# Optimization experiments

Hardware: AMD Instinct MI355X
Metric: run time of the kernel (lower is better)

The kernel has to match this reference:

```python
import jax, jax.numpy as jnp
import numpy as np

B = 1024
NOISE_DIM = 100
EMBED_DIM = 16
HIDDEN = 256
MAX_ORDER = 7
OUT_SIZE = (2 ** (MAX_ORDER + 1) + 1)  # 257
OUT_DIM = OUT_SIZE * OUT_SIZE           # 66049


def setup_inputs() -> dict:
    key = jax.random.key(0)
    ks = jax.random.split(key, 10)
    s = 0.02  # small init so sigmoid outputs are well-conditioned
    noise = jax.random.normal(ks[0], (B, NOISE_DIM), dtype=jnp.float32)
    # torch.stack in the original requires a homogeneous-order batch; use max order.
    orders = jnp.full((B,), MAX_ORDER, dtype=jnp.int32)
    embed_table = jax.random.normal(ks[1], (MAX_ORDER + 1, EMBED_DIM), dtype=jnp.float32)
    W1 = jax.random.normal(ks[2], (NOISE_DIM + EMBED_DIM, HIDDEN), dtype=jnp.float32) * s
    b1 = jnp.zeros((HIDDEN,), dtype=jnp.float32)
    W2 = jax.random.normal(ks[3], (HIDDEN, HIDDEN * 2), dtype=jnp.float32) * s
    b2 = jnp.zeros((HIDDEN * 2,), dtype=jnp.float32)
    W3 = jax.random.normal(ks[4], (HIDDEN * 2, HIDDEN * 4), dtype=jnp.float32) * s
    b3 = jnp.zeros((HIDDEN * 4,), dtype=jnp.float32)
    # expert head for the selected (homogeneous) order = MAX_ORDER
    W_out = jax.random.normal(ks[5], (HIDDEN * 4, OUT_DIM), dtype=jnp.float32) * s
    b_out = jnp.zeros((OUT_DIM,), dtype=jnp.float32)
    return {
        "noise": noise, "orders": orders, "embed_table": embed_table,
        "W1": W1, "b1": b1, "W2": W2, "b2": b2, "W3": W3, "b3": b3,
        "W_out": W_out, "b_out": b_out,
    }


def reference(noise, orders, embed_table, W1, b1, W2, b2, W3, b3, W_out, b_out):
    # embed(orders) -> (B, EMBED_DIM), concat with noise
    e = embed_table[orders]
    x = jnp.concatenate([noise, e], axis=1)            # (B, 116)
    h = jax.nn.relu(x @ W1 + b1)                       # (B, 256)
    h = jax.nn.relu(h @ W2 + b2)                       # (B, 512)
    h = jax.nn.relu(h @ W3 + b3)                       # (B, 1024)
    # per-order expert head; batch is homogeneous (all orders == MAX_ORDER),
    # the only configuration in which the original torch.stack succeeds.
    out = jax.nn.sigmoid(h @ W_out + b_out)            # (B, 66049)
    return out.reshape(noise.shape[0], OUT_SIZE, OUT_SIZE)
```

## Files before the change

kernel.cpp:

```cpp
#include <hip/hip_runtime.h>

typedef float f32x4 __attribute__((ext_vector_type(4)));
typedef float f32x2 __attribute__((ext_vector_type(2)));
typedef short s16x8 __attribute__((ext_vector_type(8)));

#define N_OUT 66049
#define K_DIM 1024
#define NPANEL 517

__device__ __forceinline__ ushort f2bf(float f) {
    union { float f; unsigned u; } x; x.f = f;
    unsigned r = x.u + 0x7fffu + ((x.u >> 16) & 1u);
    return (ushort)(r >> 16);
}

__device__ __forceinline__ unsigned cvt_pk_bf16(float lo, float hi) {
    unsigned r;
    asm("v_cvt_pk_bf16_f32 %0, %1, %2" : "=v"(r) : "v"(lo), "v"(hi));
    return r;
}

__device__ __forceinline__ void lds_load16(const void* g, void* l) {
    auto gp = reinterpret_cast<const __attribute__((address_space(1))) char*>(
        reinterpret_cast<uintptr_t>(g));
    auto lp = reinterpret_cast<__attribute__((address_space(3))) char*>(
        reinterpret_cast<uintptr_t>(l));
    __builtin_amdgcn_global_load_lds(gp, lp, 16, 0, 0);
}

__device__ __forceinline__ void chain_body(
    int bid, int tid, char* smem,
    const float* __restrict__ noise, const int* __restrict__ orders,
    const float* __restrict__ emb,
    const float* __restrict__ W1, const float* __restrict__ b1,
    const float* __restrict__ W2, const float* __restrict__ b2,
    const float* __restrict__ W3, const float* __restrict__ b3,
    ushort* __restrict__ h3)
{
    float* xs  = (float*)smem;
    float* h1s = (float*)(smem + 1920);
    float* h2s = (float*)(smem + 6016);
    const int R0 = bid * 4;

    for (int i = tid; i < 4 * 116; i += 256) {
        const int r = i / 116, c = i - r * 116;
        xs[r * 120 + c] = (c < 100) ? noise[(R0 + r) * 100 + c]
                                    : emb[orders[R0 + r] * 16 + (c - 100)];
    }
    __syncthreads();

    {
        const float bb = b1[tid];
        float a0 = bb, a1 = bb, a2 = bb, a3 = bb;
        #pragma unroll 4
        for (int k = 0; k < 116; ++k) {
            const float w = W1[k * 256 + tid];
            a0 = fmaf(xs[0 * 120 + k], w, a0);
            a1 = fmaf(xs[1 * 120 + k], w, a1);
            a2 = fmaf(xs[2 * 120 + k], w, a2);
            a3 = fmaf(xs[3 * 120 + k], w, a3);
        }
        h1s[0 * 256 + tid] = fmaxf(a0, 0.f);
        h1s[1 * 256 + tid] = fmaxf(a1, 0.f);
        h1s[2 * 256 + tid] = fmaxf(a2, 0.f);
        h1s[3 * 256 + tid] = fmaxf(a3, 0.f);
    }
    __syncthreads();

    {
        const f32x2 bb = *reinterpret_cast<const f32x2*>(&b2[tid * 2]);
        f32x2 a[4] = {bb, bb, bb, bb};
        for (int k = 0; k < 256; k += 4) {
            f32x4 hh[4];
            #pragma unroll
            for (int r = 0; r < 4; ++r) hh[r] = *reinterpret_cast<const f32x4*>(&h1s[r * 256 + k]);
            #pragma unroll
            for (int kk = 0; kk < 4; ++kk) {
                const f32x2 w = *reinterpret_cast<const f32x2*>(&W2[(k + kk) * 512 + tid * 2]);
                #pragma unroll
                for (int r = 0; r < 4; ++r) {
                    a[r][0] = fmaf(hh[r][kk], w[0], a[r][0]);
                    a[r][1] = fmaf(hh[r][kk], w[1], a[r][1]);
                }
            }
        }
        #pragma unroll
        for (int r = 0; r < 4; ++r) {
            h2s[r * 512 + tid * 2]     = fmaxf(a[r][0], 0.f);
            h2s[r * 512 + tid * 2 + 1] = fmaxf(a[r][1], 0.f);
        }
    }
    __syncthreads();

    {
        const f32x4 bb = *reinterpret_cast<const f32x4*>(&b3[tid * 4]);
        f32x4 a[4] = {bb, bb, bb, bb};
        for (int k = 0; k < 512; k += 4) {
            f32x4 hh[4];
            #pragma unroll
            for (int r = 0; r < 4; ++r) hh[r] = *reinterpret_cast<const f32x4*>(&h2s[r * 512 + k]);
            #pragma unroll
            for (int kk = 0; kk < 4; ++kk) {
                const f32x4 w = *reinterpret_cast<const f32x4*>(&W3[(k + kk) * 1024 + tid * 4]);
                #pragma unroll
                for (int r = 0; r < 4; ++r) {
                    a[r][0] = fmaf(hh[r][kk], w[0], a[r][0]);
                    a[r][1] = fmaf(hh[r][kk], w[1], a[r][1]);
                    a[r][2] = fmaf(hh[r][kk], w[2], a[r][2]);
                    a[r][3] = fmaf(hh[r][kk], w[3], a[r][3]);
                }
            }
        }
        #pragma unroll
        for (int r = 0; r < 4; ++r) {
            ushort4 u;
            u.x = f2bf(fmaxf(a[r][0], 0.f));
            u.y = f2bf(fmaxf(a[r][1], 0.f));
            u.z = f2bf(fmaxf(a[r][2], 0.f));
            u.w = f2bf(fmaxf(a[r][3], 0.f));
            *reinterpret_cast<ushort4*>(&h3[(size_t)(R0 + r) * 1024 + tid * 4]) = u;
        }
    }
}

__device__ __forceinline__ void convert_wout_body(
    int p, int kt, int tid, char* smem,
    const float* __restrict__ Wout, ushort* __restrict__ Bp)
{
    float* T = (float*)smem;
    const int k0 = kt * 64;

    if (p < NPANEL - 1) {
        const int c4 = (tid & 31) * 4;
        const int r0 = tid >> 5;
        const float* src = Wout + (size_t)k0 * N_OUT + (size_t)p * 128 + c4;
        #pragma unroll
        for (int i = 0; i < 8; ++i) {
            const int r = r0 + i * 8;
            f32x4 v = __builtin_nontemporal_load(
                reinterpret_cast<const f32x4*>(src + (size_t)r * N_OUT));
            *reinterpret_cast<f32x4*>(&T[r * 132 + c4]) = v;
        }
    } else {
        const int c = tid & 31, r0 = tid >> 5;
        #pragma unroll
        for (int i = 0; i < 8; ++i) {
            const int r = r0 + i * 8;
            #pragma unroll
            for (int j = 0; j < 4; ++j) {
                int col = p * 128 + c * 4 + j;
                if (col > N_OUT - 1) col = N_OUT - 1;
                T[r * 132 + c * 4 + j] = Wout[(size_t)(k0 + r) * N_OUT + col];
            }
        }
    }
    __syncthreads();

    const size_t base = ((size_t)p * 128 + kt * 8) * 128 * 8;
    #pragma unroll
    for (int i = 0; i < 4; ++i) {
        const int v = tid + i * 256;
        const int kbl = v >> 7, nl = v & 127;
        s16x8 o;
        #pragma unroll
        for (int j = 0; j < 8; ++j) o[j] = (short)f2bf(T[(kbl * 8 + j) * 132 + nl]);
        *reinterpret_cast<s16x8*>(Bp + base + (size_t)v * 8) = o;
    }
}

__global__ __launch_bounds__(256) void prep(
    const float* __restrict__ noise, const int* __restrict__ orders,
    const float* __restrict__ emb,
    const float* __restrict__ W1, const float* __restrict__ b1,
    const float* __restrict__ W2, const float* __restrict__ b2,
    const float* __restrict__ W3, const float* __restrict__ b3,
    const float* __restrict__ Wout,
    ushort* __restrict__ h3, ushort* __restrict__ Bp)
{
    __shared__ __align__(16) char smem[33792];
    const int bx = blockIdx.x;
    const int tid = threadIdx.x;
    if (bx < 256) {
        chain_body(bx, tid, smem, noise, orders, emb, W1, b1, W2, b2, W3, b3, h3);
    } else {
        const int c = bx - 256;
        const int p  = c % NPANEL;
        const int kt = c / NPANEL;
        convert_wout_body(p, kt, tid, smem, Wout, Bp);
    }
}

__global__ __launch_bounds__(256, 3) void gemm_out(
    const ushort* __restrict__ h3, const ushort* __restrict__ Bp,
    const float* __restrict__ bout, float* __restrict__ out)
{
    __shared__ __align__(16) char smem[33792];
    ushort* Alds = (ushort*)smem;

    const int tid = threadIdx.x;
    const int lane = tid & 63;
    const int w = tid >> 6;
    const int wm = w >> 1, wn = w & 1;
    const int u4 = lane >> 4, l15 = lane & 15;

    const int raw = blockIdx.x;
    const int panel = (raw >> 6) * 8 + (raw & 7);
    const int mblk = (raw >> 3) & 7;
    if (panel >= NPANEL) return;
    const int m0 = mblk * 128;
    const int n0 = panel * 128;

    f32x4 acc[4][4] = {};
    s16x8 bfr[4][2];

    const int arow = wm * 64 + l15;
    const int bn   = wn * 64 + l15;

    const ushort* BpPanel = Bp + (size_t)panel * (128 * 128 * 8);
    const ushort* Bth = BpPanel + ((size_t)(u4 << 7) + bn) * 8;

    auto stageA = [&](int kt) {
        const int k0 = kt * 64;
        #pragma unroll
        for (int i = 0; i < 4; ++i) {
            const int u = (w * 4 + i) * 64 + lane;
            const int r = u >> 3, cc = u & 7;
            const ushort* src = h3 + (((size_t)(m0 + r)) << 10) + (k0 + ((cc ^ (r & 7)) << 3));
            lds_load16(src, (void*)&Alds[(w * 4 + i) * 512]);
        }
    };
    auto loadB = [&](int kt) {
        const ushort* t0 = Bth + (size_t)kt * 8192;
        #pragma unroll
        for (int ks = 0; ks < 2; ++ks)
            #pragma unroll
            for (int fn = 0; fn < 4; ++fn)
                bfr[fn][ks] = *reinterpret_cast<const s16x8*>(t0 + ks * 4096 + fn * 128);
    };
    auto compute = [&]() {
        #pragma unroll
        for (int ks = 0; ks < 2; ++ks) {
            s16x8 af[4];
            #pragma unroll
            for (int fm = 0; fm < 4; ++fm) {
                const int r = arow + fm * 16;
                const int cc = (ks * 4 + u4) ^ (r & 7);
                af[fm] = *reinterpret_cast<const s16x8*>(&Alds[r * 64 + cc * 8]);
            }
            #pragma unroll
            for (int fm = 0; fm < 4; ++fm)
                #pragma unroll
                for (int fn = 0; fn < 4; ++fn)
                    acc[fm][fn] = __builtin_amdgcn_mfma_f32_16x16x32_bf16(
                        af[fm], bfr[fn][ks], acc[fm][fn], 0, 0, 0);
        }
    };

    stageA(0);
    __builtin_amdgcn_sched_barrier(0);
    loadB(0);
    __builtin_amdgcn_sched_barrier(0);
    asm volatile("s_waitcnt vmcnt(8)" ::: "memory");
    asm volatile("s_barrier" ::: "memory");

    for (int kt = 0; kt < 16; ++kt) {
        compute();
        asm volatile("s_waitcnt lgkmcnt(0)" ::: "memory");
        asm volatile("s_barrier" ::: "memory");
        if (kt < 15) {
            stageA(kt + 1);
            __builtin_amdgcn_sched_barrier(0);
            loadB(kt + 1);
            __builtin_amdgcn_sched_barrier(0);
            asm volatile("s_waitcnt vmcnt(8)" ::: "memory");
            asm volatile("s_barrier" ::: "memory");
        }
    }

    if (n0 + 128 <= N_OUT) {
        float bo[4];
        #pragma unroll
        for (int fn = 0; fn < 4; ++fn) bo[fn] = bout[n0 + wn * 64 + fn * 16 + l15];
        float* Elds = (float*)smem;
        #pragma unroll
        for (int p = 0; p < 2; ++p) {
            if (wm == p) {
                #pragma unroll
                for (int fm = 0; fm < 4; ++fm)
                    #pragma unroll
                    for (int fn = 0; fn < 4; ++fn)
                        #pragma unroll
                        for (int j = 0; j < 4; ++j) {
                            const int rl = fm * 16 + u4 * 4 + j;
                            const int cl = wn * 64 + fn * 16 + l15;
                            const float z = acc[fm][fn][j] + bo[fn];
                            Elds[rl * 132 + cl] = 1.f / (1.f + __expf(-z));
                        }
            }
            __syncthreads();
            const size_t gb = (size_t)(m0 + p * 64) * N_OUT + n0;
            const int g = tid >> 5, c4 = (tid & 31) * 4;
            #pragma unroll
            for (int i = 0; i < 8; ++i) {
                const int rl = i * 8 + g;
                const f32x4 v = *reinterpret_cast<const f32x4*>(&Elds[rl * 132 + c4]);
                __builtin_nontemporal_store(v,
                    reinterpret_cast<f32x4*>(&out[gb + (size_t)rl * N_OUT + c4]));
            }
            __syncthreads();
        }
    } else {
        const int rbase = m0 + wm * 64 + u4 * 4;
        #pragma unroll
        for (int fn = 0; fn < 4; ++fn) {
            const int col = n0 + wn * 64 + fn * 16 + l15;
            const bool ok = col < N_OUT;
            const float bo = bout[ok ? col : (N_OUT - 1)];
            #pragma unroll
            for (int fm = 0; fm < 4; ++fm) {
                #pragma unroll
                for (int j = 0; j < 4; ++j) {
                    if (ok) {
                        const int row = rbase + fm * 16 + j;
                        const float z = acc[fm][fn][j] + bo;
                        out[(size_t)row * N_OUT + col] = 1.f / (1.f + __expf(-z));
                    }
                }
            }
        }
    }
}

__global__ __launch_bounds__(256) void gemm_out_fused(
    const ushort* __restrict__ h3, const float* __restrict__ Wout,
    const float* __restrict__ bout, float* __restrict__ out)
{
    __shared__ __align__(16) char smem[33792];
    ushort* Alds = (ushort*)smem;
    ushort* Blds = (ushort*)(smem + 16384);

    const int tid = threadIdx.x;
    const int lane = tid & 63;
    const int w = tid >> 6;
    const int wm = w >> 1, wn = w & 1;

    const int raw = blockIdx.x;
    const int panel = (raw >> 6) * 8 + (raw & 7);
    const int mblk = (raw >> 3) & 7;
    if (panel >= NPANEL) return;
    const int m0 = mblk * 128;
    const int n0 = panel * 128;

    const int nl = tid & 127;
    const int kb0 = tid >> 7;
    int nc = n0 + nl; if (nc > N_OUT - 1) nc = N_OUT - 1;
    const float* Bsrc = Wout + nc;

    f32x4 acc[4][4] = {};
    float breg[32];

    const int arow = wm * 64 + (lane & 15);
    const int ac0  = lane >> 4;
    const int bn   = wn * 64 + (lane & 15);

    auto stageA = [&](int kt) {
        const int k0 = kt * 64;
        #pragma unroll
        for (int i = 0; i < 4; ++i) {
            const int u = (w * 4 + i) * 64 + lane;
            const int r = u >> 3, cc = u & 7;
            const ushort* src = h3 + (size_t)(m0 + r) * K_DIM + (k0 + ((cc ^ (r & 7)) << 3));
            lds_load16(src, (void*)&Alds[(w * 4 + i) * 512]);
        }
    };
    auto loadB = [&](int kt) {
        const int k0 = kt * 64;
        #pragma unroll
        for (int g = 0; g < 4; ++g) {
            const int kb = kb0 + g * 2;
            #pragma unroll
            for (int i = 0; i < 8; ++i)
                breg[g * 8 + i] = Bsrc[(size_t)(k0 + kb * 8 + i) * N_OUT];
        }
    };
    auto writeB = [&]() {
        #pragma unroll
        for (int g = 0; g < 4; ++g) {
            const int kb = kb0 + g * 2;
            union { s16x8 v; unsigned u[4]; } pk;
            #pragma unroll
            for (int h = 0; h < 4; ++h)
                pk.u[h] = cvt_pk_bf16(breg[g * 8 + 2 * h], breg[g * 8 + 2 * h + 1]);
            *reinterpret_cast<s16x8*>(&Blds[(kb * 128 + nl) * 8]) = pk.v;
        }
    };
    auto compute = [&]() {
        #pragma unroll
        for (int ks = 0; ks < 2; ++ks) {
            s16x8 af[4], bfr[4];
            #pragma unroll
            for (int fm = 0; fm < 4; ++fm) {
                const int r = arow + fm * 16;
                const int cc = (ks * 4 + ac0) ^ (r & 7);
                af[fm] = *reinterpret_cast<const s16x8*>(&Alds[r * 64 + cc * 8]);
            }
            const int kb = ks * 4 + ac0;
            #pragma unroll
            for (int fn = 0; fn < 4; ++fn)
                bfr[fn] = *reinterpret_cast<const s16x8*>(&Blds[(kb * 128 + bn + fn * 16) * 8]);
            #pragma unroll
            for (int fm = 0; fm < 4; ++fm)
                #pragma unroll
                for (int fn = 0; fn < 4; ++fn)
                    acc[fm][fn] = __builtin_amdgcn_mfma_f32_16x16x32_bf16(
                        af[fm], bfr[fn], acc[fm][fn], 0, 0, 0);
        }
    };

    stageA(0);
    loadB(0);
    asm volatile("s_waitcnt vmcnt(0)" ::: "memory");
    asm volatile("s_barrier" ::: "memory");
    writeB();
    loadB(1);
    asm volatile("s_waitcnt lgkmcnt(0)" ::: "memory");
    asm volatile("s_barrier" ::: "memory");

    for (int kt = 0; kt < 16; ++kt) {
        compute();
        asm volatile("s_barrier" ::: "memory");
        if (kt < 15) {
            stageA(kt + 1);
            __builtin_amdgcn_sched_barrier(0);
            writeB();
            if (kt < 14) {
                loadB(kt + 2);
                asm volatile("s_waitcnt lgkmcnt(0)" ::: "memory");
                asm volatile("s_waitcnt vmcnt(32)" ::: "memory");
            } else {
                asm volatile("s_waitcnt lgkmcnt(0)" ::: "memory");
                asm volatile("s_waitcnt vmcnt(0)" ::: "memory");
            }
            asm volatile("s_barrier" ::: "memory");
        }
    }

    if (n0 + 128 <= N_OUT) {
        float bo[4];
        #pragma unroll
        for (int fn = 0; fn < 4; ++fn) bo[fn] = bout[n0 + wn * 64 + fn * 16 + (lane & 15)];
        float* Elds = (float*)smem;
        #pragma unroll
        for (int p = 0; p < 2; ++p) {
            if (wm == p) {
                #pragma unroll
                for (int fm = 0; fm < 4; ++fm)
                    #pragma unroll
                    for (int fn = 0; fn < 4; ++fn)
                        #pragma unroll
                        for (int j = 0; j < 4; ++j) {
                            const int rl = fm * 16 + (lane >> 4) * 4 + j;
                            const int cl = wn * 64 + fn * 16 + (lane & 15);
                            const float z = acc[fm][fn][j] + bo[fn];
                            Elds[rl * 132 + cl] = 1.f / (1.f + __expf(-z));
                        }
            }
            __syncthreads();
            const size_t gb = (size_t)(m0 + p * 64) * N_OUT + n0;
            const int g = tid >> 5, c4 = (tid & 31) * 4;
            #pragma unroll
            for (int i = 0; i < 8; ++i) {
                const int rl = i * 8 + g;
                const f32x4 v = *reinterpret_cast<const f32x4*>(&Elds[rl * 132 + c4]);
                *reinterpret_cast<f32x4*>(&out[gb + (size_t)rl * N_OUT + c4]) = v;
            }
            __syncthreads();
        }
    } else {
        const int rbase = m0 + wm * 64 + (lane >> 4) * 4;
        #pragma unroll
        for (int fn = 0; fn < 4; ++fn) {
            const int col = n0 + wn * 64 + fn * 16 + (lane & 15);
            const bool ok = col < N_OUT;
            const float bo = bout[ok ? col : (N_OUT - 1)];
            #pragma unroll
            for (int fm = 0; fm < 4; ++fm) {
                #pragma unroll
                for (int j = 0; j < 4; ++j) {
                    if (ok) {
                        const int row = rbase + fm * 16 + j;
                        const float z = acc[fm][fn][j] + bo;
                        out[(size_t)row * N_OUT + col] = 1.f / (1.f + __expf(-z));
                    }
                }
            }
        }
    }
}

extern "C" void kernel_launch(void* const* d_in, const int* in_sizes, int n_in,
                              void* d_out, int out_size, void* d_ws, size_t ws_size,
                              hipStream_t stream)
{
    const float* noise = (const float*)d_in[0];
    const int*   orders = (const int*)d_in[1];
    const float* emb   = (const float*)d_in[2];
    const float* W1 = (const float*)d_in[3];
    const float* b1 = (const float*)d_in[4];
    const float* W2 = (const float*)d_in[5];
    const float* b2 = (const float*)d_in[6];
    const float* W3 = (const float*)d_in[7];
    const float* b3 = (const float*)d_in[8];
    const float* Wout = (const float*)d_in[9];
    const float* bout = (const float*)d_in[10];

    char* ws = (char*)d_ws;
    ushort* h3 = (ushort*)ws;
    ushort* Bp = (ushort*)(ws + 0x200000);
    const size_t need = 0x200000 + (size_t)NPANEL * 128 * 128 * 8 * 2;
    const bool pre = (ws_size >= need);

    if (pre) {
        prep<<<256 + NPANEL * 16, 256, 0, stream>>>(
            noise, orders, emb, W1, b1, W2, b2, W3, b3, Wout, h3, Bp);
        gemm_out<<<4160, 256, 0, stream>>>(h3, Bp, bout, (float*)d_out);
    } else {
        prep<<<256, 256, 0, stream>>>(
            noise, orders, emb, W1, b1, W2, b2, W3, b3, Wout, h3, Bp);
        gemm_out_fused<<<4160, 256, 0, stream>>>(h3, Wout, bout, (float*)d_out);
    }
}
```

Before: 310.9 us.

## Load A fragments directly from global into registers with double-buffered prefetch

Drops LDS staging of the activation tile and its barriers in the output GEMM. Each wave now reads its A and B fragments straight from global memory into registers, using a two-stage register double buffer so loads for the next k-slice are in flight while the MFMAs for the current one run. This removes LDS traffic and synchronisation, but A rows are no longer shared through LDS, so each wave re-reads them from global or cache, and register pressure goes up.

```diff
diff --git a/kernel.cpp b/kernel.cpp
--- a/kernel.cpp
+++ b/kernel.cpp
@@ -195,7 +195,6 @@
     const float* __restrict__ bout, float* __restrict__ out)
 {
     __shared__ __align__(16) char smem[33792];
-    ushort* Alds = (ushort*)smem;
 
     const int tid = threadIdx.x;
     const int lane = tid & 63;
@@ -211,70 +210,44 @@
     const int n0 = panel * 128;
 
     f32x4 acc[4][4] = {};
-    s16x8 bfr[4][2];
 
     const int arow = wm * 64 + l15;
     const int bn   = wn * 64 + l15;
 
-    const ushort* BpPanel = Bp + (size_t)panel * (128 * 128 * 8);
-    const ushort* Bth = BpPanel + ((size_t)(u4 << 7) + bn) * 8;
-
-    auto stageA = [&](int kt) {
-        const int k0 = kt * 64;
-        #pragma unroll
-        for (int i = 0; i < 4; ++i) {
-            const int u = (w * 4 + i) * 64 + lane;
-            const int r = u >> 3, cc = u & 7;
-            const ushort* src = h3 + (((size_t)(m0 + r)) << 10) + (k0 + ((cc ^ (r & 7)) << 3));
-            lds_load16(src, (void*)&Alds[(w * 4 + i) * 512]);
-        }
+    const ushort* ap0 = h3 + ((size_t)(m0 + arow) << 10) + u4 * 8;
+    const ushort* ap1 = ap0 + (16 << 10);
+    const ushort* ap2 = ap0 + (32 << 10);
+    const ushort* ap3 = ap0 + (48 << 10);
+    const ushort* bp  = Bp + (size_t)panel * (128 * 128 * 8) + u4 * 1024 + bn * 8;
+
+    s16x8 a0[4], b0[4], a1[4], b1[4];
+
+    auto LD = [&](int s, s16x8* A, s16x8* B) {
+        const int ao = s * 32;
+        A[0] = *reinterpret_cast<const s16x8*>(ap0 + ao);
+        A[1] = *reinterpret_cast<const s16x8*>(ap1 + ao);
+        A[2] = *reinterpret_cast<const s16x8*>(ap2 + ao);
+        A[3] = *reinterpret_cast<const s16x8*>(ap3 + ao);
+        const ushort* bs = bp + (size_t)s * 4096;
+        #pragma unroll
+        for (int fn = 0; fn < 4; ++fn)
+            B[fn] = *reinterpret_cast<const s16x8*>(bs + fn * 128);
     };
-    auto loadB = [&](int kt) {
-        const ushort* t0 = Bth + (size_t)kt * 8192;
-        #pragma unroll
-        for (int ks = 0; ks < 2; ++ks)
+    auto MM = [&](s16x8* A, s16x8* B) {
+        #pragma unroll
+        for (int fm = 0; fm < 4; ++fm)
             #pragma unroll
             for (int fn = 0; fn < 4; ++fn)
-                bfr[fn][ks] = *reinterpret_cast<const s16x8*>(t0 + ks * 4096 + fn * 128);
+                acc[fm][fn] = __builtin_amdgcn_mfma_f32_16x16x32_bf16(
+                    A[fm], B[fn], acc[fm][fn], 0, 0, 0);
     };
-    auto compute = [&]() {
-        #pragma unroll
-        for (int ks = 0; ks < 2; ++ks) {
-            s16x8 af[4];
-            #pragma unroll
-            for (int fm = 0; fm < 4; ++fm) {
-                const int r = arow + fm * 16;
-                const int cc = (ks * 4 + u4) ^ (r & 7);
-                af[fm] = *reinterpret_cast<const s16x8*>(&Alds[r * 64 + cc * 8]);
-            }
-            #pragma unroll
-            for (int fm = 0; fm < 4; ++fm)
-                #pragma unroll
-                for (int fn = 0; fn < 4; ++fn)
-                    acc[fm][fn] = __builtin_amdgcn_mfma_f32_16x16x32_bf16(
-                        af[fm], bfr[fn][ks], acc[fm][fn], 0, 0, 0);
-        }
-    };
-
-    stageA(0);
-    __builtin_amdgcn_sched_barrier(0);
-    loadB(0);
-    __builtin_amdgcn_sched_barrier(0);
-    asm volatile("s_waitcnt vmcnt(8)" ::: "memory");
-    asm volatile("s_barrier" ::: "memory");
-
-    for (int kt = 0; kt < 16; ++kt) {
-        compute();
-        asm volatile("s_waitcnt lgkmcnt(0)" ::: "memory");
-        asm volatile("s_barrier" ::: "memory");
-        if (kt < 15) {
-            stageA(kt + 1);
-            __builtin_amdgcn_sched_barrier(0);
-            loadB(kt + 1);
-            __builtin_amdgcn_sched_barrier(0);
-            asm volatile("s_waitcnt vmcnt(8)" ::: "memory");
-            asm volatile("s_barrier" ::: "memory");
-        }
+
+    LD(0, a0, b0);
+    for (int s = 0; s < 32; s += 2) {
+        if (s + 1 < 32) LD(s + 1, a1, b1);
+        MM(a0, b0);
+        if (s + 2 < 32) LD(s + 2, a0, b0);
+        if (s + 1 < 32) MM(a1, b1);
     }
 
     if (n0 + 128 <= N_OUT) {
```

After: 485.1 us. +56.0%, slower.
